# Optimization experiments

Measured on AMD Instinct MI355X. Metric: run time of the kernel, lower is better.

## Reference

```python
import jax, jax.numpy as jnp
import numpy as np

STRIDES = (4, 8, 16, 32, 64)
RATIOS = (0.5, 1.0, 2.0)
SCALE = 8.0
A = 3
PRE_NMS = 2000
MAX_PER_IMG = 1000
NMS_THR = 0.7
MAX_RATIO = float(abs(np.log(16.0 / 1000.0)))  # wh_ratio_clip = 16/1000
LEVEL_OFFSET = 4096.0  # > max image coordinate, separates levels for batched NMS
FEAT_HW = ((208, 336), (104, 168), (52, 84), (26, 42), (13, 21))
N = 8


def grid_anchors(stride, H, W):
    # mmdet-style base anchors: scale 8, ratios (0.5,1,2), centered at 0
    r = jnp.asarray(RATIOS, jnp.float32)
    h_r = jnp.sqrt(r)
    w_r = 1.0 / h_r
    ws = stride * w_r * SCALE
    hs = stride * h_r * SCALE
    base = jnp.stack([-ws / 2, -hs / 2, ws / 2, hs / 2], axis=-1)  # [A,4]
    sx = jnp.arange(W, dtype=jnp.float32) * stride
    sy = jnp.arange(H, dtype=jnp.float32) * stride
    yy, xx = jnp.meshgrid(sy, sx, indexing='ij')
    shifts = jnp.stack([xx, yy, xx, yy], axis=-1).reshape(-1, 4)  # [H*W,4], row-major
    return (shifts[:, None, :] + base[None, :, :]).reshape(-1, 4)  # [H*W*A,4]


def decode(anchors, deltas, h, w):
    # DeltaXYWH decode with means 0, stds 1, clip to image
    px = (anchors[..., 0] + anchors[..., 2]) * 0.5
    py = (anchors[..., 1] + anchors[..., 3]) * 0.5
    pw = anchors[..., 2] - anchors[..., 0]
    ph = anchors[..., 3] - anchors[..., 1]
    dx, dy = deltas[..., 0], deltas[..., 1]
    dw = jnp.clip(deltas[..., 2], -MAX_RATIO, MAX_RATIO)
    dh = jnp.clip(deltas[..., 3], -MAX_RATIO, MAX_RATIO)
    gx = px + pw * dx
    gy = py + ph * dy
    gw = pw * jnp.exp(dw)
    gh = ph * jnp.exp(dh)
    x1 = jnp.clip(gx - gw * 0.5, 0.0, w)
    y1 = jnp.clip(gy - gh * 0.5, 0.0, h)
    x2 = jnp.clip(gx + gw * 0.5, 0.0, w)
    y2 = jnp.clip(gy + gh * 0.5, 0.0, h)
    return jnp.stack([x1, y1, x2, y2], axis=-1)


def iou_matrix(b):
    area = (b[:, 2] - b[:, 0]) * (b[:, 3] - b[:, 1])
    lt = jnp.maximum(b[:, None, :2], b[None, :, :2])
    rb = jnp.minimum(b[:, None, 2:], b[None, :, 2:])
    wh = jnp.clip(rb - lt, 0.0, None)
    inter = wh[..., 0] * wh[..., 1]
    union = area[:, None] + area[None, :] - inter
    return inter / jnp.maximum(union, 1e-6)


def _forward(cls_list, reg_list, image_h, image_w):
    scores_all, deltas_all, anchors_all, levels_all = [], [], [], []
    for lvl, (cls, reg) in enumerate(zip(cls_list, reg_list)):
        n, _, H, W = cls.shape
        anchors = grid_anchors(STRIDES[lvl], H, W)  # [H*W*A,4]
        s = jax.nn.sigmoid(jnp.transpose(cls, (0, 2, 3, 1)).reshape(n, -1))
        d = jnp.transpose(reg, (0, 2, 3, 1)).reshape(n, -1, 4)
        k = min(PRE_NMS, s.shape[1])  # topk pre-selection per level
        sv, si = jax.lax.top_k(s, k)
        dv = jnp.take_along_axis(d, si[..., None], axis=1)
        av = anchors[si]
        scores_all.append(sv)
        deltas_all.append(dv)
        anchors_all.append(av)
        levels_all.append(jnp.full((k,), lvl, jnp.int32))
    scores = jnp.concatenate(scores_all, axis=1)    # [N,M]
    deltas = jnp.concatenate(deltas_all, axis=1)    # [N,M,4]
    anchors = jnp.concatenate(anchors_all, axis=1)  # [N,M,4]
    levels = jnp.concatenate(levels_all)            # [M] (same per image)
    boxes = decode(anchors, deltas, float(image_h), float(image_w))
    # filter_boxes with min_area = prod((0,0)) = 0: keep boxes with area >= 0
    area = (boxes[..., 2] - boxes[..., 0]) * (boxes[..., 3] - boxes[..., 1])
    scores = jnp.where(area >= 0.0, scores, -1.0)
    M = boxes.shape[1]
    idxs = jnp.arange(M)

    def nms_one(bs):
        b_i, s_i = bs
        order = jnp.argsort(-s_i)
        b = b_i[order]
        s = s_i[order]
        lv = levels[order]
        # batched NMS: offset each level so cross-level boxes never overlap
        ob = jax.lax.stop_gradient(b + (lv.astype(b.dtype) * LEVEL_OFFSET)[:, None])
        iou = iou_matrix(ob)  # [M,M]

        def body(i, keep):
            sup = (iou[i] > NMS_THR) & (idxs > i) & keep[i]
            return keep & (~sup)

        keep = jax.lax.fori_loop(0, M, body, jnp.ones((M,), bool))
        rank = jnp.cumsum(keep.astype(jnp.int32)) - 1
        tgt = jnp.where(keep & (rank < MAX_PER_IMG), rank, MAX_PER_IMG)  # dump slot
        out_b = jnp.zeros((MAX_PER_IMG + 1, 4), b.dtype).at[tgt].set(b)[:MAX_PER_IMG]
        out_s = jnp.zeros((MAX_PER_IMG + 1,), s.dtype).at[tgt].set(s)[:MAX_PER_IMG]
        return out_b, out_s

    pb, ps = jax.lax.map(nms_one, (boxes, scores))  # sequential per image
    return pb, ps  # [N,1000,4], [N,1000] (zero-padded)


def setup_inputs() -> dict:
    key = jax.random.key(0)
    inp = {}
    for lvl, (H, W) in enumerate(FEAT_HW):
        k1 = jax.random.fold_in(key, 2 * lvl)
        k2 = jax.random.fold_in(key, 2 * lvl + 1)
        inp[f"class_out_{lvl}"] = jax.random.normal(k1, (N, A, H, W), jnp.float32)
        inp[f"reg_out_{lvl}"] = jax.random.normal(k2, (N, 4 * A, H, W), jnp.float32)
    inp["image_h"] = 832
    inp["image_w"] = 1344
    return inp


def reference(class_out_0, class_out_1, class_out_2, class_out_3, class_out_4,
              reg_out_0, reg_out_1, reg_out_2, reg_out_3, reg_out_4,
              image_h, image_w):
    cls_list = [class_out_0, class_out_1, class_out_2, class_out_3, class_out_4]
    reg_list = [reg_out_0, reg_out_1, reg_out_2, reg_out_3, reg_out_4]
    return _forward(cls_list, reg_list, image_h, image_w)
```

## Files before the change

### kernel.cpp

```cpp
#include <hip/hip_runtime.h>
#include <cmath>

#pragma clang fp contract(off)

namespace {
constexpr int NIMG = 8;
constexpr int NLVL = 5;
constexpr int LH[5]   = {208,104,52,26,13};
constexpr int LW[5]   = {336,168,84,42,21};
constexpr int LSTR[5] = {4,8,16,32,64};
constexpr int HWA[5]  = {209664,52416,13104,3276,819};
constexpr int KSEL[5] = {2000,2000,2000,2000,819};
constexpr int SOFF[5] = {0,2000,4000,6000,8000};
constexpr int MTOT    = 8819;
constexpr int CAP     = 6144;
constexpr int NPAIR   = NIMG*NLVL;
constexpr int CCUM[5] = {52,65,69,70,71};
constexpr int BLK_PER_IMG = 71;
constexpr int MASK_W  = 32;
constexpr int OUTK    = 1000;
constexpr int NT2[5]  = {272,272,272,272,55};

constexpr size_t OFF_HIST   = 0;
constexpr size_t OFF_PKC    = 0;
constexpr size_t OFF_CNT    = 655360;
constexpr size_t OFF_THR    = 655520;
constexpr size_t ZERO_BYTES = 655680;
constexpr size_t OFF_CAND   = 655872;
constexpr size_t OFF_SELKEY = 1921120;
constexpr size_t OFF_SELSC  = 2485536;
constexpr size_t OFF_SELBOX = 2767744;
constexpr size_t OFF_MASK   = 3896576;
constexpr size_t OFF_CKEY   = OFF_MASK;
constexpr size_t OFF_KEEP   = 24376576;
}

struct Ins {
  const float* cls[5];
  const float* reg[5];
  const int* ih;
  const int* iw;
};

__device__ __forceinline__ void decode_block(int b, int& img, int& lvl, int& chunk) {
  img = b / BLK_PER_IMG;
  int rb = b - img*BLK_PER_IMG;
  if      (rb < CCUM[0]) { lvl=0; chunk=rb; }
  else if (rb < CCUM[1]) { lvl=1; chunk=rb-CCUM[0]; }
  else if (rb < CCUM[2]) { lvl=2; chunk=rb-CCUM[1]; }
  else if (rb < CCUM[3]) { lvl=3; chunk=rb-CCUM[2]; }
  else                   { lvl=4; chunk=0; }
}

__device__ __forceinline__ unsigned mapbits(float x) {
  unsigned u = __float_as_uint(x);
  return u ^ (unsigned)(((int)u >> 31) | (int)0x80000000);
}

__device__ __forceinline__ float sigmoid_ref(float x) {
  float e = (float)exp(-(double)x);
  return 1.0f / (1.0f + e);
}

__global__ void k_hist(Ins in, unsigned* __restrict__ hist) {
  int img, lvl, chunk; decode_block(blockIdx.x, img, lvl, chunk);
  __shared__ unsigned lh[4096];
  for (int i = threadIdx.x; i < 4096; i += 256) lh[i] = 0;
  __syncthreads();
  const float* src = in.cls[lvl] + (size_t)img * HWA[lvl];
  if (lvl != 4) {
    const float4* src4 = (const float4*)src;
    int nf4 = HWA[lvl] >> 2;
    int base4 = chunk * 1024;
    #pragma unroll
    for (int j = 0; j < 4; j++) {
      int f = base4 + j*256 + threadIdx.x;
      if (f < nf4) {
        float4 v = src4[f];
        atomicAdd(&lh[mapbits(v.x) >> 20], 1u);
        atomicAdd(&lh[mapbits(v.y) >> 20], 1u);
        atomicAdd(&lh[mapbits(v.z) >> 20], 1u);
        atomicAdd(&lh[mapbits(v.w) >> 20], 1u);
      }
    }
  } else {
    int base = chunk * 4096;
    #pragma unroll
    for (int j = 0; j < 16; j++) {
      int e = base + j*256 + threadIdx.x;
      if (e < HWA[4]) atomicAdd(&lh[mapbits(src[e]) >> 20], 1u);
    }
  }
  __syncthreads();
  unsigned* gh = hist + (img*NLVL + lvl) * 4096;
  for (int i = threadIdx.x; i < 4096; i += 256)
    if (lh[i]) atomicAdd(&gh[i], lh[i]);
}

__global__ void k_scan(const unsigned* __restrict__ hist, unsigned* __restrict__ thr) {
  int pair = blockIdx.x; int lvl = pair % NLVL;
  const unsigned* h = hist + (size_t)pair * 4096;
  __shared__ unsigned part[256];
  unsigned s = 0;
  #pragma unroll
  for (int i = 0; i < 16; i++) s += h[threadIdx.x*16 + i];
  part[threadIdx.x] = s;
  __syncthreads();
  if (threadIdx.x == 0) {
    unsigned k = (unsigned)KSEL[lvl];
    unsigned cum = 0;
    unsigned edge = 0;
    for (int t = 255; t >= 0; t--) {
      if (cum + part[t] >= k) {
        for (int b = t*16 + 15; b >= t*16; b--) {
          cum += h[b];
          if (cum >= k) { edge = (unsigned)b; break; }
        }
        thr[pair] = edge << 20;
        return;
      }
      cum += part[t];
    }
    thr[pair] = 0u;
  }
}

__global__ void __launch_bounds__(256) k_compact(Ins in, const unsigned* __restrict__ thr,
                          unsigned* __restrict__ cnt, unsigned* __restrict__ cand,
                          unsigned long long* __restrict__ ckey) {
  int img, lvl, chunk; decode_block(blockIdx.x, img, lvl, chunk);
  int pair = img*NLVL + lvl;
  unsigned T = thr[pair];
  const float* src = in.cls[lvl] + (size_t)img * HWA[lvl];
  int hw = LH[lvl] * LW[lvl];
  int lid = threadIdx.x & 63;
  __shared__ unsigned lbuf[4096];
  __shared__ unsigned long long lkey[4096];
  __shared__ unsigned lc, gbase;
  if (threadIdx.x == 0) lc = 0;
  __syncthreads();

  auto emit = [&](int e, float v, bool sel) {
    unsigned long long mask = __ballot(sel);
    if (mask != 0ull) {
      int leader = __ffsll((long long)mask) - 1;
      unsigned wb = 0;
      if (lid == leader) wb = atomicAdd(&lc, (unsigned)__popcll(mask));
      wb = (unsigned)__shfl((int)wb, leader, 64);
      if (sel) {
        unsigned p = wb + (unsigned)__popcll(mask & ((1ull << lid) - 1ull));
        int a = e / hw;
        int r = e - a*hw;
        unsigned idx = (unsigned)(r*3 + a);
        lbuf[p] = idx;
        float s = sigmoid_ref(v);
        unsigned pack = ((unsigned)lvl << 18) | idx;
        lkey[p] = ((unsigned long long)__float_as_uint(s) << 21)
                | (unsigned long long)(0x1FFFFFu - pack);
      }
    }
  };

  if (lvl != 4) {
    const float4* src4 = (const float4*)src;
    int nf4 = HWA[lvl] >> 2;
    int base4 = chunk * 1024;
    #pragma unroll
    for (int j = 0; j < 4; j++) {
      int f = base4 + j*256 + threadIdx.x;
      bool inb = f < nf4;
      float4 v4 = make_float4(0.f, 0.f, 0.f, 0.f);
      if (inb) v4 = src4[f];
      int e0 = f * 4;
      emit(e0+0, v4.x, inb && (mapbits(v4.x) >= T));
      emit(e0+1, v4.y, inb && (mapbits(v4.y) >= T));
      emit(e0+2, v4.z, inb && (mapbits(v4.z) >= T));
      emit(e0+3, v4.w, inb && (mapbits(v4.w) >= T));
    }
  } else {
    int base = chunk * 4096;
    #pragma unroll
    for (int j = 0; j < 16; j++) {
      int e = base + j*256 + threadIdx.x;
      float v = 0.0f;
      bool inb = (e < HWA[4]);
      if (inb) v = src[e];
      emit(e, v, inb && (mapbits(v) >= T));
    }
  }
  __syncthreads();
  if (threadIdx.x == 0) gbase = atomicAdd(&cnt[pair], lc);
  __syncthreads();
  unsigned nsel = lc, gb = gbase;
  for (unsigned t = threadIdx.x; t < nsel; t += 256) {
    unsigned p = gb + t;
    if (p < CAP) {
      cand[(size_t)pair*CAP + p] = lbuf[t];
      ckey[(size_t)pair*CAP + p] = lkey[t];
    }
  }
}

__global__ void __launch_bounds__(256) k_rank(Ins in, const unsigned* __restrict__ cntA,
                       const unsigned* __restrict__ cand,
                       const unsigned long long* __restrict__ ckey,
                       unsigned long long* __restrict__ sel_key,
                       float* __restrict__ sel_sc,
                       float* __restrict__ sel_box) {
  int pair = blockIdx.y; int tile = blockIdx.x;
  int img = pair / NLVL, lvl = pair % NLVL;
  int c = min((int)cntA[pair], CAP);
  if (tile*256 >= c) return;
  const unsigned long long* kp = ckey + (size_t)pair*CAP;
  int jj = tile*256 + threadIdx.x;
  bool act = jj < c;
  unsigned long long mykey = kp[min(jj, c-1)];
  int lane = threadIdx.x & 63;
  int rk = 0;

  auto window = [&](int w0, bool tail) {
    const ulonglong2* kp2 = (const ulonglong2*)(kp + w0);
    ulonglong2 A = kp2[lane];
    ulonglong2 B = kp2[64 + lane];
    if (tail) {
      int i = w0 + 2*lane;
      if (i     >= c) A.x = 0ull;
      if (i + 1 >= c) A.y = 0ull;
      if (i + 128 >= c) B.x = 0ull;
      if (i + 129 >= c) B.y = 0ull;
    }
    #pragma unroll
    for (int mk = 0; mk < 64; mk++) {
      unsigned mlo = (unsigned)__builtin_amdgcn_readlane((int)(unsigned)mykey, mk);
      unsigned mhi = (unsigned)__builtin_amdgcn_readlane((int)(unsigned)(mykey >> 32), mk);
      unsigned long long smk = ((unsigned long long)mhi << 32) | (unsigned long long)mlo;
      int add = __popcll(__ballot(A.x > smk)) + __popcll(__ballot(A.y > smk))
              + __popcll(__ballot(B.x > smk)) + __popcll(__ballot(B.y > smk));
      if (lane == mk) rk += add;
    }
  };

  int nfull = c >> 8;
  for (int w = 0; w < nfull; w++) window(w*256, false);
  if (c & 255) window(nfull*256, true);

  if (act && rk < KSEL[lvl]) {
    int slot = img*MTOT + SOFF[lvl] + rk;
    sel_key[slot] = mykey;
    sel_sc[slot]  = __uint_as_float((unsigned)(mykey >> 21));
    unsigned idx = cand[(size_t)pair*CAP + jj];
    int a = (int)(idx % 3u);
    int r = (int)(idx / 3u);
    int Wl = LW[lvl]; int hw = LH[lvl]*Wl;
    int x = r % Wl, y = r / Wl;
    const float* rg = in.reg[lvl] + (size_t)img * 4 * HWA[lvl];
    float dx = rg[(a*4+0)*hw + r];
    float dy = rg[(a*4+1)*hw + r];
    float dw = rg[(a*4+2)*hw + r];
    float dh = rg[(a*4+3)*hw + r];
    float ratio = (a==0) ? 0.5f : (a==1) ? 1.0f : 2.0f;
    float hr = sqrtf(ratio);
    float wr = 1.0f / hr;
    float st = (float)LSTR[lvl];
    float wsz = st * wr * 8.0f;
    float hsz = st * hr * 8.0f;
    float xs = (float)x * st, ys = (float)y * st;
    float x1 = xs - wsz*0.5f, x2 = xs + wsz*0.5f;
    float y1 = ys - hsz*0.5f, y2 = ys + hsz*0.5f;
    float px = (x1 + x2) * 0.5f, py = (y1 + y2) * 0.5f;
    float pw = x2 - x1,          ph = y2 - y1;
    const float MR = 4.135166556742356f;
    dw = fminf(fmaxf(dw, -MR), MR);
    dh = fminf(fmaxf(dh, -MR), MR);
    float gx = px + pw*dx, gy = py + ph*dy;
    float gw = pw * (float)exp((double)dw);
    float gh = ph * (float)exp((double)dh);
    float Wi = (float)(*in.iw), Hi = (float)(*in.ih);
    float4 bb;
    bb.x = fminf(fmaxf(gx - gw*0.5f, 0.0f), Wi);
    bb.y = fminf(fmaxf(gy - gh*0.5f, 0.0f), Hi);
    bb.z = fminf(fmaxf(gx + gw*0.5f, 0.0f), Wi);
    bb.w = fminf(fmaxf(gy + gh*0.5f, 0.0f), Hi);
    ((float4*)sel_box)[slot] = bb;
  }
}

__global__ void __launch_bounds__(256) k_masks(const float* __restrict__ sel_box,
                        unsigned long long* __restrict__ maskbuf) {
  int pair = blockIdx.y; int lvl = pair % NLVL; int img = pair / NLVL;
  int n = KSEL[lvl];
  int nw = (n + 63) >> 6;
  int nwc2 = (nw + 1) >> 1;
  int wv = threadIdx.x >> 6;
  int lane = threadIdx.x & 63;
  int t = blockIdx.x * 4 + wv;
  if (t >= NT2[lvl]) return;
  int rb = 0, cum = 0;
  while (cum + (nwc2 - (rb >> 1)) <= t) { cum += nwc2 - (rb >> 1); rb++; }
  int jw2 = (rb >> 1) + (t - cum);
  int jw0 = 2*jw2, jw1 = jw0 + 1;
  const float4* boxes = ((const float4*)sel_box) + img*MTOT + SOFF[lvl];
  float off = (float)lvl * 4096.0f;
  int c0 = jw0*64 + lane, c1 = c0 + 64;
  float b0x,b0y,b0z,b0w,a0, b1x,b1y,b1z,b1w,a1;
  if (c0 < n) {
    float4 b = boxes[c0];
    b0x = b.x + off; b0y = b.y + off; b0z = b.z + off; b0w = b.w + off;
    a0 = (b0z - b0x) * (b0w - b0y);
  } else { b0x=b0y=b0z=b0w=3.0e8f; a0=0.0f; }
  if (c1 < n) {
    float4 b = boxes[c1];
    b1x = b.x + off; b1y = b.y + off; b1z = b.z + off; b1w = b.w + off;
    a1 = (b1z - b1x) * (b1w - b1y);
  } else { b1x=b1y=b1z=b1w=3.0e8f; a1=0.0f; }
  __shared__ float4 sbox[4][64];
  __shared__ float  sarea[4][64];
  int row0 = rb*64;
  {
    float4 bi0 = boxes[min(row0 + lane, n-1)];
    bi0.x += off; bi0.y += off; bi0.z += off; bi0.w += off;
    sbox[wv][lane] = bi0;
    sarea[wv][lane] = (bi0.z - bi0.x) * (bi0.w - bi0.y);
  }
  bool z0 = (jw0 < rb);
  bool d0 = (jw0 == rb), d1 = (jw1 == rb);
  const float CHI = 0x1.66666ap-1f;
  const float CLO = 0x1.666664p-1f;
  unsigned long long acc0 = 0ull, acc1 = 0ull, unc = 0ull;
  #pragma unroll 16
  for (int r = 0; r < 64; r++) {
    float4 bi = sbox[wv][r];
    float ai = sarea[wv][r];
    float xx1 = fmaxf(bi.x, b0x), yy1 = fmaxf(bi.y, b0y);
    float xx2 = fminf(bi.z, b0z), yy2 = fminf(bi.w, b0w);
    float iw_ = fmaxf(xx2 - xx1, 0.0f), ih_ = fmaxf(yy2 - yy1, 0.0f);
    float in0 = iw_ * ih_;
    float u0 = fmaxf((ai + a0) - in0, 1e-6f);
    float xc1 = fmaxf(bi.x, b1x), yc1 = fmaxf(bi.y, b1y);
    float xc2 = fminf(bi.z, b1z), yc2 = fminf(bi.w, b1w);
    float jw_ = fmaxf(xc2 - xc1, 0.0f), jh_ = fmaxf(yc2 - yc1, 0.0f);
    float in1 = jw_ * jh_;
    float u1 = fmaxf((ai + a1) - in1, 1e-6f);
    unsigned long long h0 = __ballot(in0 >= CHI * u0);
    unsigned long long l0 = __ballot(in0 >= CLO * u0);
    unsigned long long h1 = __ballot(in1 >= CHI * u1);
    unsigned long long l1 = __ballot(in1 >= CLO * u1);
    unc |= (h0 ^ l0) | (h1 ^ l1);
    unsigned long long dm = ~((2ull << r) - 1ull);
    unsigned long long m0 = z0 ? 0ull : (d0 ? (h0 & dm) : h0);
    unsigned long long m1 = d1 ? (h1 & dm) : h1;
    if (lane == r) { acc0 = m0; acc1 = m1; }
  }
  if (unc) {
    const double Md = 0.70000001788139343261718750;
    acc0 = 0ull; acc1 = 0ull;
    #pragma unroll 1
    for (int r = 0; r < 64; r++) {
      float4 bi = sbox[wv][r];
      float ai = sarea[wv][r];
      float xx1 = fmaxf(bi.x, b0x), yy1 = fmaxf(bi.y, b0y);
      float xx2 = fminf(bi.z, b0z), yy2 = fminf(bi.w, b0w);
      float iw_ = fmaxf(xx2 - xx1, 0.0f), ih_ = fmaxf(yy2 - yy1, 0.0f);
      float in0 = iw_ * ih_;
      float u0 = fmaxf((ai + a0) - in0, 1e-6f);
      float xc1 = fmaxf(bi.x, b1x), yc1 = fmaxf(bi.y, b1y);
      float xc2 = fminf(bi.z, b1z), yc2 = fminf(bi.w, b1w);
      float jw_ = fmaxf(xc2 - xc1, 0.0f), jh_ = fmaxf(yc2 - yc1, 0.0f);
      float in1 = jw_ * jh_;
      float u1 = fmaxf((ai + a1) - in1, 1e-6f);
      unsigned long long w0 = __ballot((double)in0 >= Md * (double)u0);
      unsigned long long w1 = __ballot((double)in1 >= Md * (double)u1);
      unsigned long long dm = ~((2ull << r) - 1ull);
      unsigned long long m0 = z0 ? 0ull : (d0 ? (w0 & dm) : w0);
      unsigned long long m1 = d1 ? (w1 & dm) : w1;
      if (lane == r) { acc0 = m0; acc1 = m1; }
    }
  }
  int row = row0 + lane;
  if (row < n) {
    unsigned long long* dst = maskbuf + (size_t)pair*2000*MASK_W + (size_t)row*MASK_W + jw0;
    if (z0) {
      dst[1] = acc1;
    } else {
      ulonglong2 v; v.x = acc0; v.y = acc1;
      *((ulonglong2*)dst) = v;
    }
  }
}

__global__ void __launch_bounds__(1024) k_nms(const unsigned long long* __restrict__ maskbuf,
                      unsigned long long* __restrict__ keep, int* __restrict__ pkc) {
  int pair = blockIdx.x; int lvl = pair % NLVL;
  int n = KSEL[lvl];
  int nw = (n + 63) >> 6;
  const unsigned long long* mrow = maskbuf + (size_t)pair*2000*MASK_W;
  int tid = threadIdx.x;
  int w  = tid & 31;
  int rg = tid >> 5;
  __shared__ unsigned long long rem[32];
  __shared__ unsigned long long diag[64];
  __shared__ unsigned long long skw[32];
  __shared__ unsigned long long sSk;
  __shared__ int lcnt[64];
  if (tid < 32) { rem[tid] = 0ull; skw[tid] = 0ull; }
  __syncthreads();

  unsigned long long A0, A1, B0, B1;
  {
    int r0 = min(rg*2, n-1), r1 = min(rg*2+1, n-1);
    A0 = mrow[(size_t)r0*MASK_W + w];
    A1 = mrow[(size_t)r1*MASK_W + w];
  }
  for (int k = 0; k < nw; k++) {
    if (k + 1 < nw) {
      int r0 = min(64*(k+1) + rg*2, n-1), r1 = min(64*(k+1) + rg*2 + 1, n-1);
      B0 = mrow[(size_t)r0*MASK_W + w];
      B1 = mrow[(size_t)r1*MASK_W + w];
    }
    if (w == k) { diag[rg*2] = A0; diag[rg*2+1] = A1; }
    __syncthreads();
    if (tid < 64) {
      int row = 64*k + tid;
      bool valid = row < n;
      unsigned long long D = valid ? diag[tid] : 0ull;
      unsigned long long rk = rem[k];
      unsigned long long S = rk;
      for (int it = 0; it < 64; it++) {
        bool kept = valid && !((S >> tid) & 1ull);
        unsigned long long c = kept ? D : 0ull;
        #pragma unroll
        for (int m = 1; m < 64; m <<= 1) {
          unsigned lo = (unsigned)__shfl_xor((int)(unsigned)(c & 0xffffffffull), m, 64);
          unsigned hi = (unsigned)__shfl_xor((int)(unsigned)(c >> 32), m, 64);
          c |= ((unsigned long long)hi << 32) | (unsigned long long)lo;
        }
        unsigned long long Snew = rk | c;
        if (Snew == S) break;
        S = Snew;
      }
      if (tid == 0) {
        sSk = S;
        int nb = n - 64*k;
        unsigned long long vm = (nb >= 64) ? ~0ull : ((1ull << nb) - 1ull);
        unsigned long long kw = (~S) & vm;
        skw[k] = kw;
        keep[(size_t)pair*MASK_W + k] = kw;
      }
    }
    __syncthreads();
    if (w > k) {
      unsigned long long Sk = sSk;
      int r0 = 64*k + rg*2, r1 = r0 + 1;
      unsigned long long m = 0ull;
      if (r0 < n && !((Sk >> (rg*2)) & 1ull))     m |= A0;
      if (r1 < n && !((Sk >> (rg*2+1)) & 1ull))   m |= A1;
      if (m) atomicOr(&rem[w], m);
    }
    __syncthreads();
    A0 = B0; A1 = B1;
  }
  if (tid < 64) {
    int lane = tid;
    unsigned long long kw = (lane < nw) ? skw[lane] : 0ull;
    lcnt[lane] = __popcll(kw);
    int pre = 0;
    for (int t2 = 0; t2 < lane; t2++) pre += lcnt[t2];
    for (int b = 0; b < 64; b++) {
      int p = lane*64 + b;
      if (p < n) {
        pre += (int)((kw >> b) & 1ull);
        pkc[pair*2048 + p] = pre;
      }
    }
  }
}

__global__ void __launch_bounds__(256) k_out2(const unsigned long long* __restrict__ sel_key,
                      const float* __restrict__ sel_box,
                      const unsigned long long* __restrict__ keep,
                      const int* __restrict__ pkc,
                      float* __restrict__ out) {
  int img = blockIdx.y;
  int pos = blockIdx.x*256 + threadIdx.x;
  if (pos >= MTOT) return;
  int lvl = pos<2000?0 : pos<4000?1 : pos<6000?2 : pos<8000?3 : 4;
  int local = pos - SOFF[lvl];
  int pair = img*NLVL + lvl;
  unsigned long long kw = keep[(size_t)pair*MASK_W + (local >> 6)];
  if (!((kw >> (local & 63)) & 1ull)) return;
  unsigned long long mykey = sel_key[img*MTOT + pos];
  int rank = pkc[pair*2048 + local] - 1;
  #pragma unroll
  for (int l2 = 0; l2 < NLVL; l2++) {
    if (l2 == lvl) continue;
    const unsigned long long* A = sel_key + img*MTOT + SOFF[l2];
    int lo = 0, hi = KSEL[l2];
    while (lo < hi) {
      int mid = (lo + hi) >> 1;
      if (A[mid] > mykey) lo = mid + 1; else hi = mid;
    }
    if (lo > 0) rank += pkc[(img*NLVL + l2)*2048 + lo - 1];
  }
  if (rank < OUTK) {
    ((float4*)out)[img*OUTK + rank] = ((const float4*)sel_box)[img*MTOT + pos];
    out[NIMG*OUTK*4 + img*OUTK + rank] = __uint_as_float((unsigned)(mykey >> 21));
  }
}

extern "C" void kernel_launch(void* const* d_in, const int* in_sizes, int n_in,
                              void* d_out, int out_size, void* d_ws, size_t ws_size,
                              hipStream_t stream) {
  Ins in;
  for (int l = 0; l < 5; l++) {
    in.cls[l] = (const float*)d_in[2*l];
    in.reg[l] = (const float*)d_in[2*l + 1];
  }
  in.ih = (const int*)d_in[10];
  in.iw = (const int*)d_in[11];

  char* ws = (char*)d_ws;
  unsigned* hist              = (unsigned*)(ws + OFF_HIST);
  int* pkc                    = (int*)(ws + OFF_PKC);
  unsigned* cnt               = (unsigned*)(ws + OFF_CNT);
  unsigned* thr               = (unsigned*)(ws + OFF_THR);
  unsigned* cand              = (unsigned*)(ws + OFF_CAND);
  unsigned long long* sel_key = (unsigned long long*)(ws + OFF_SELKEY);
  float* sel_sc               = (float*)(ws + OFF_SELSC);
  float* sel_box              = (float*)(ws + OFF_SELBOX);
  unsigned long long* maskbuf = (unsigned long long*)(ws + OFF_MASK);
  unsigned long long* ckey    = (unsigned long long*)(ws + OFF_CKEY);
  unsigned long long* keep    = (unsigned long long*)(ws + OFF_KEEP);
  float* out                  = (float*)d_out;

  hipMemsetAsync(d_ws, 0, ZERO_BYTES, stream);
  hipMemsetAsync(d_out, 0, (size_t)NIMG*OUTK*5*sizeof(float), stream);

  k_hist   <<<NIMG*BLK_PER_IMG, 256, 0, stream>>>(in, hist);
  k_scan   <<<NPAIR, 256, 0, stream>>>(hist, thr);
  k_compact<<<NIMG*BLK_PER_IMG, 256, 0, stream>>>(in, thr, cnt, cand, ckey);
  k_rank   <<<dim3(CAP/256, NPAIR), 256, 0, stream>>>(in, cnt, cand, ckey, sel_key, sel_sc, sel_box);
  k_masks  <<<dim3(68, NPAIR), 256, 0, stream>>>(sel_box, maskbuf);
  k_nms    <<<NPAIR, 1024, 0, stream>>>(maskbuf, keep, pkc);
  k_out2   <<<dim3((MTOT + 255)/256, NIMG), 256, 0, stream>>>(sel_key, sel_box, keep, pkc, out);
}
```

Before: 268.8 us.

## Decode boxes during compaction and simplify rank to scalar key comparisons

Box decoding moves from the rank kernel into the compaction kernel, so every candidate's box is computed once and written to a per-pair candidate box buffer. The rank kernel then only copies the precomputed box for selected candidates, and the candidate-index and score arrays are dropped. The ballot/readlane wavefront rank loop is replaced by a plain per-thread loop over all keys with four accumulators, relying on uniform broadcast loads. This decodes every candidate above the threshold rather than only those selected, and the scalar rank loop may be slower than the ballot-based comparison.

```diff
diff --git a/kernel.cpp b/kernel.cpp
--- a/kernel.cpp
+++ b/kernel.cpp
@@ -26,12 +26,11 @@
 constexpr size_t OFF_CNT    = 655360;
 constexpr size_t OFF_THR    = 655520;
 constexpr size_t ZERO_BYTES = 655680;
-constexpr size_t OFF_CAND   = 655872;
 constexpr size_t OFF_SELKEY = 1921120;
-constexpr size_t OFF_SELSC  = 2485536;
 constexpr size_t OFF_SELBOX = 2767744;
 constexpr size_t OFF_MASK   = 3896576;
 constexpr size_t OFF_CKEY   = OFF_MASK;
+constexpr size_t OFF_CBOX   = OFF_MASK + 2097152;
 constexpr size_t OFF_KEEP   = 24376576;
 }
 
@@ -126,8 +125,9 @@
 }
 
 __global__ void __launch_bounds__(256) k_compact(Ins in, const unsigned* __restrict__ thr,
-                          unsigned* __restrict__ cnt, unsigned* __restrict__ cand,
-                          unsigned long long* __restrict__ ckey) {
+                          unsigned* __restrict__ cnt,
+                          unsigned long long* __restrict__ ckey,
+                          float4* __restrict__ cbox) {
   int img, lvl, chunk; decode_block(blockIdx.x, img, lvl, chunk);
   int pair = img*NLVL + lvl;
   unsigned T = thr[pair];
@@ -192,20 +192,52 @@
   if (threadIdx.x == 0) gbase = atomicAdd(&cnt[pair], lc);
   __syncthreads();
   unsigned nsel = lc, gb = gbase;
+  float Wi = (float)(*in.iw), Hi = (float)(*in.ih);
+  int Wl = LW[lvl];
+  float st = (float)LSTR[lvl];
+  const float* rg = in.reg[lvl] + (size_t)img * 4 * HWA[lvl];
   for (unsigned t = threadIdx.x; t < nsel; t += 256) {
     unsigned p = gb + t;
     if (p < CAP) {
-      cand[(size_t)pair*CAP + p] = lbuf[t];
+      unsigned idx = lbuf[t];
       ckey[(size_t)pair*CAP + p] = lkey[t];
-    }
-  }
-}
-
-__global__ void __launch_bounds__(256) k_rank(Ins in, const unsigned* __restrict__ cntA,
-                       const unsigned* __restrict__ cand,
+      int a = (int)(idx % 3u);
+      int r = (int)(idx / 3u);
+      int x = r % Wl, y = r / Wl;
+      float dx = rg[(a*4+0)*hw + r];
+      float dy = rg[(a*4+1)*hw + r];
+      float dwv = rg[(a*4+2)*hw + r];
+      float dhv = rg[(a*4+3)*hw + r];
+      float ratio = (a==0) ? 0.5f : (a==1) ? 1.0f : 2.0f;
+      float hr = sqrtf(ratio);
+      float wr = 1.0f / hr;
+      float wsz = st * wr * 8.0f;
+      float hsz = st * hr * 8.0f;
+      float xs = (float)x * st, ys = (float)y * st;
+      float x1 = xs - wsz*0.5f, x2 = xs + wsz*0.5f;
+      float y1 = ys - hsz*0.5f, y2 = ys + hsz*0.5f;
+      float px = (x1 + x2) * 0.5f, py = (y1 + y2) * 0.5f;
+      float pw = x2 - x1,          ph = y2 - y1;
+      const float MR = 4.135166556742356f;
+      dwv = fminf(fmaxf(dwv, -MR), MR);
+      dhv = fminf(fmaxf(dhv, -MR), MR);
+      float gx = px + pw*dx, gy = py + ph*dy;
+      float gw = pw * (float)exp((double)dwv);
+      float gh = ph * (float)exp((double)dhv);
+      float4 bb;
+      bb.x = fminf(fmaxf(gx - gw*0.5f, 0.0f), Wi);
+      bb.y = fminf(fmaxf(gy - gh*0.5f, 0.0f), Hi);
+      bb.z = fminf(fmaxf(gx + gw*0.5f, 0.0f), Wi);
+      bb.w = fminf(fmaxf(gy + gh*0.5f, 0.0f), Hi);
+      cbox[(size_t)pair*CAP + p] = bb;
+    }
+  }
+}
+
+__global__ void __launch_bounds__(256) k_rank(const unsigned* __restrict__ cntA,
                        const unsigned long long* __restrict__ ckey,
+                       const float4* __restrict__ cbox,
                        unsigned long long* __restrict__ sel_key,
-                       float* __restrict__ sel_sc,
                        float* __restrict__ sel_box) {
   int pair = blockIdx.y; int tile = blockIdx.x;
   int img = pair / NLVL, lvl = pair % NLVL;
@@ -215,73 +247,23 @@
   int jj = tile*256 + threadIdx.x;
   bool act = jj < c;
   unsigned long long mykey = kp[min(jj, c-1)];
-  int lane = threadIdx.x & 63;
-  int rk = 0;
-
-  auto window = [&](int w0, bool tail) {
-    const ulonglong2* kp2 = (const ulonglong2*)(kp + w0);
-    ulonglong2 A = kp2[lane];
-    ulonglong2 B = kp2[64 + lane];
-    if (tail) {
-      int i = w0 + 2*lane;
-      if (i     >= c) A.x = 0ull;
-      if (i + 1 >= c) A.y = 0ull;
-      if (i + 128 >= c) B.x = 0ull;
-      if (i + 129 >= c) B.y = 0ull;
-    }
+  int c_r = c & ~15;
+  int r0 = 0, r1 = 0, r2 = 0, r3 = 0;
+  for (int j0 = 0; j0 < c_r; j0 += 16) {
     #pragma unroll
-    for (int mk = 0; mk < 64; mk++) {
-      unsigned mlo = (unsigned)__builtin_amdgcn_readlane((int)(unsigned)mykey, mk);
-      unsigned mhi = (unsigned)__builtin_amdgcn_readlane((int)(unsigned)(mykey >> 32), mk);
-      unsigned long long smk = ((unsigned long long)mhi << 32) | (unsigned long long)mlo;
-      int add = __popcll(__ballot(A.x > smk)) + __popcll(__ballot(A.y > smk))
-              + __popcll(__ballot(B.x > smk)) + __popcll(__ballot(B.y > smk));
-      if (lane == mk) rk += add;
-    }
-  };
-
-  int nfull = c >> 8;
-  for (int w = 0; w < nfull; w++) window(w*256, false);
-  if (c & 255) window(nfull*256, true);
-
+    for (int u = 0; u < 16; u += 4) {
+      r0 += (kp[j0+u  ] > mykey) ? 1 : 0;
+      r1 += (kp[j0+u+1] > mykey) ? 1 : 0;
+      r2 += (kp[j0+u+2] > mykey) ? 1 : 0;
+      r3 += (kp[j0+u+3] > mykey) ? 1 : 0;
+    }
+  }
+  int rk = r0 + r1 + r2 + r3;
+  for (int j = c_r; j < c; j++) rk += (kp[j] > mykey) ? 1 : 0;
   if (act && rk < KSEL[lvl]) {
     int slot = img*MTOT + SOFF[lvl] + rk;
     sel_key[slot] = mykey;
-    sel_sc[slot]  = __uint_as_float((unsigned)(mykey >> 21));
-    unsigned idx = cand[(size_t)pair*CAP + jj];
-    int a = (int)(idx % 3u);
-    int r = (int)(idx / 3u);
-    int Wl = LW[lvl]; int hw = LH[lvl]*Wl;
-    int x = r % Wl, y = r / Wl;
-    const float* rg = in.reg[lvl] + (size_t)img * 4 * HWA[lvl];
-    float dx = rg[(a*4+0)*hw + r];
-    float dy = rg[(a*4+1)*hw + r];
-    float dw = rg[(a*4+2)*hw + r];
-    float dh = rg[(a*4+3)*hw + r];
-    float ratio = (a==0) ? 0.5f : (a==1) ? 1.0f : 2.0f;
-    float hr = sqrtf(ratio);
-    float wr = 1.0f / hr;
-    float st = (float)LSTR[lvl];
-    float wsz = st * wr * 8.0f;
-    float hsz = st * hr * 8.0f;
-    float xs = (float)x * st, ys = (float)y * st;
-    float x1 = xs - wsz*0.5f, x2 = xs + wsz*0.5f;
-    float y1 = ys - hsz*0.5f, y2 = ys + hsz*0.5f;
-    float px = (x1 + x2) * 0.5f, py = (y1 + y2) * 0.5f;
-    float pw = x2 - x1,          ph = y2 - y1;
-    const float MR = 4.135166556742356f;
-    dw = fminf(fmaxf(dw, -MR), MR);
-    dh = fminf(fmaxf(dh, -MR), MR);
-    float gx = px + pw*dx, gy = py + ph*dy;
-    float gw = pw * (float)exp((double)dw);
-    float gh = ph * (float)exp((double)dh);
-    float Wi = (float)(*in.iw), Hi = (float)(*in.ih);
-    float4 bb;
-    bb.x = fminf(fmaxf(gx - gw*0.5f, 0.0f), Wi);
-    bb.y = fminf(fmaxf(gy - gh*0.5f, 0.0f), Hi);
-    bb.z = fminf(fmaxf(gx + gw*0.5f, 0.0f), Wi);
-    bb.w = fminf(fmaxf(gy + gh*0.5f, 0.0f), Hi);
-    ((float4*)sel_box)[slot] = bb;
+    ((float4*)sel_box)[slot] = cbox[(size_t)pair*CAP + jj];
   }
 }
 
@@ -523,12 +505,11 @@
   int* pkc                    = (int*)(ws + OFF_PKC);
   unsigned* cnt               = (unsigned*)(ws + OFF_CNT);
   unsigned* thr               = (unsigned*)(ws + OFF_THR);
-  unsigned* cand              = (unsigned*)(ws + OFF_CAND);
   unsigned long long* sel_key = (unsigned long long*)(ws + OFF_SELKEY);
-  float* sel_sc               = (float*)(ws + OFF_SELSC);
   float* sel_box              = (float*)(ws + OFF_SELBOX);
   unsigned long long* maskbuf = (unsigned long long*)(ws + OFF_MASK);
   unsigned long long* ckey    = (unsigned long long*)(ws + OFF_CKEY);
+  float4* cbox                = (float4*)(ws + OFF_CBOX);
   unsigned long long* keep    = (unsigned long long*)(ws + OFF_KEEP);
   float* out                  = (float*)d_out;
 
@@ -537,8 +518,8 @@
 
   k_hist   <<<NIMG*BLK_PER_IMG, 256, 0, stream>>>(in, hist);
   k_scan   <<<NPAIR, 256, 0, stream>>>(hist, thr);
-  k_compact<<<NIMG*BLK_PER_IMG, 256, 0, stream>>>(in, thr, cnt, cand, ckey);
-  k_rank   <<<dim3(CAP/256, NPAIR), 256, 0, stream>>>(in, cnt, cand, ckey, sel_key, sel_sc, sel_box);
+  k_compact<<<NIMG*BLK_PER_IMG, 256, 0, stream>>>(in, thr, cnt, ckey, cbox);
+  k_rank   <<<dim3(CAP/256, NPAIR), 256, 0, stream>>>(cnt, ckey, cbox, sel_key, sel_box);
   k_masks  <<<dim3(68, NPAIR), 256, 0, stream>>>(sel_box, maskbuf);
   k_nms    <<<NPAIR, 1024, 0, stream>>>(maskbuf, keep, pkc);
   k_out2   <<<dim3((MTOT + 255)/256, NIMG), 256, 0, stream>>>(sel_key, sel_box, keep, pkc, out);
```

Measured after the change: 286.8 us. 6.7% more time.
